# Performance work log

Measured on AMD Instinct MI355X. Metric: run time of the kernel, lower is better.

Reference implementation:

```python
import jax, jax.numpy as jnp
import numpy as np

N_HEAD = 16
N_KV_HEAD = 8
HEAD_DIM = 128
N_EMBED = 2048
EPS = 1.1920929e-07  # torch default eps for fp32 rms_norm


def _apply_rotary_emb(x, cos, sin):
    # x: (B, T, H, D); cos/sin: (1, T, 1, D//2)  (nanochat-style half rotation)
    d = x.shape[-1] // 2
    x1, x2 = x[..., :d], x[..., d:]
    y1 = x1 * cos + x2 * sin
    y2 = -x1 * sin + x2 * cos
    return jnp.concatenate([y1, y2], axis=-1).astype(x.dtype)


def _rms_norm(x):
    return x * jax.lax.rsqrt(jnp.mean(jnp.square(x), axis=-1, keepdims=True) + EPS)


def setup_inputs() -> dict:
    key = jax.random.key(0)
    ks = jax.random.split(key, 5)
    B, T = 2, 2048
    kv_dim = N_KV_HEAD * HEAD_DIM
    x = jax.random.normal(ks[0], (B, T, N_EMBED), dtype=jnp.float32)
    w_attn = jax.random.normal(ks[1], (N_EMBED + 2 * kv_dim, N_EMBED), dtype=jnp.float32) * 0.02
    w_proj = jax.random.normal(ks[2], (N_EMBED, N_EMBED), dtype=jnp.float32) * 0.02
    # realistic RoPE tables
    half = HEAD_DIM // 2
    inv_freq = 1.0 / (10000.0 ** (jnp.arange(half, dtype=jnp.float32) / half))
    freqs = jnp.arange(T, dtype=jnp.float32)[:, None] * inv_freq[None, :]  # (T, half)
    cos = jnp.cos(freqs)[None, :, None, :]
    sin = jnp.sin(freqs)[None, :, None, :]
    return {"x": x, "w_attn": w_attn, "w_proj": w_proj, "cos": cos, "sin": sin}


def reference(x, w_attn, w_proj, cos, sin):
    B, T, C = x.shape
    kv_dim = N_KV_HEAD * HEAD_DIM
    qkv = jnp.einsum('btc,oc->bto', x, w_attn)  # (B, T, C + 2*kv_dim)
    q = qkv[..., :C].reshape(B, T, N_HEAD, HEAD_DIM)
    k = qkv[..., C:C + kv_dim].reshape(B, T, N_KV_HEAD, HEAD_DIM)
    v = qkv[..., C + kv_dim:].reshape(B, T, N_KV_HEAD, HEAD_DIM)
    q = _rms_norm(_apply_rotary_emb(q, cos, sin))
    k = _rms_norm(_apply_rotary_emb(k, cos, sin))
    # GQA: repeat kv heads to match query heads
    rep = N_HEAD // N_KV_HEAD
    k = jnp.repeat(k, rep, axis=2)  # (B, T, n_head, D)
    v = jnp.repeat(v, rep, axis=2)
    scale = 1.0 / jnp.sqrt(jnp.float32(HEAD_DIM))
    scores = jnp.einsum('bqhd,bkhd->bhqk', q, k) * scale  # (B, H, T, T)
    causal = jnp.tril(jnp.ones((T, T), dtype=bool))
    scores = jnp.where(causal[None, None], scores, jnp.finfo(scores.dtype).min)
    attn = jax.nn.softmax(scores, axis=-1)
    y = jnp.einsum('bhqk,bkhd->bqhd', attn, v).reshape(B, T, C)
    return jnp.einsum('btc,oc->bto', y, w_proj)
```

## Files before the change

kernel.cpp:

```cpp
#include <hip/hip_runtime.h>

#define B_ 2
#define T_ 2048
#define NH 16
#define NKV 8
#define HD 128
#define C_ 2048
#define KVD (NKV*HD)
#define QKVD (C_ + 2*KVD)
#define NTOK (B_*T_)

typedef __bf16 bf16_t;
typedef __bf16 bf16x4_t __attribute__((ext_vector_type(4)));
typedef __bf16 bf16x8_t __attribute__((ext_vector_type(8)));
typedef float f32x4_t __attribute__((ext_vector_type(4)));
typedef float f32x16_t __attribute__((ext_vector_type(16)));

__device__ __forceinline__ f32x4_t mfma16(bf16x8_t a, bf16x8_t b, f32x4_t c) {
  return __builtin_amdgcn_mfma_f32_16x16x32_bf16(a, b, c, 0, 0, 0);
}
__device__ __forceinline__ f32x16_t mfma32(bf16x8_t a, bf16x8_t b, f32x16_t c) {
  return __builtin_amdgcn_mfma_f32_32x32x16_bf16(a, b, c, 0, 0, 0);
}
__device__ __forceinline__ f32x16_t zero16() {
  f32x16_t z;
  #pragma unroll
  for (int i = 0; i < 16; i++) z[i] = 0.f;
  return z;
}

#define GLDS16(gp, lp) __builtin_amdgcn_global_load_lds( \
    (const __attribute__((address_space(1))) void*)(gp), \
    (__attribute__((address_space(3))) void*)(lp), 16, 0, 0)

__global__ __launch_bounds__(256) void cvt3_kernel(const float* __restrict__ s0, bf16_t* __restrict__ d0,
                                                   const float* __restrict__ s1, bf16_t* __restrict__ d1,
                                                   const float* __restrict__ s2, bf16_t* __restrict__ d2) {
  int bid = blockIdx.x;
  const float* s; bf16_t* d; int off;
  if (bid < 8192)       { s = s0; d = d0; off = bid; }
  else if (bid < 16384) { s = s1; d = d1; off = bid - 8192; }
  else                  { s = s2; d = d2; off = bid - 16384; }
  int i = (off * 256 + threadIdx.x) * 4;
  const float4 v = *(const float4*)(s + i);
  bf16x4_t o;
  o[0] = (bf16_t)v.x; o[1] = (bf16_t)v.y; o[2] = (bf16_t)v.z; o[3] = (bf16_t)v.w;
  *(bf16x4_t*)(d + i) = o;
}

__global__ void gemm_nt(const bf16_t* __restrict__ A, const bf16_t* __restrict__ Bm,
                        float* __restrict__ Cf, bf16_t* __restrict__ Cb, int M, int N, int K) {
  __shared__ bf16_t As[128*32];
  __shared__ bf16_t Bs[128*32];
  int tid = threadIdx.x;
  int wave = tid >> 6, lane = tid & 63;
  int quad = lane >> 4, l16 = lane & 15;
  int wm = (wave >> 1) * 64, wn = (wave & 1) * 64;
  int bm = blockIdx.y * 128, bn = blockIdx.x * 128;
  int grow = wave * 32 + (lane >> 2);
  int gcol = (lane & 3) * 8;
  const bf16_t* pa = A + (size_t)(bm + grow) * K + gcol;
  const bf16_t* pb = Bm + (size_t)(bn + grow) * K + gcol;
  bf16_t* lA0 = &As[(wave * 32) * 32];
  bf16_t* lA1 = &As[(wave * 32 + 16) * 32];
  bf16_t* lB0 = &Bs[(wave * 32) * 32];
  bf16_t* lB1 = &Bs[(wave * 32 + 16) * 32];
  f32x4_t acc[4][4];
  #pragma unroll
  for (int i = 0; i < 4; i++)
    #pragma unroll
    for (int j = 0; j < 4; j++) acc[i][j] = (f32x4_t){0.f,0.f,0.f,0.f};
  for (int k0 = 0; k0 < K; k0 += 32) {
    __syncthreads();
    GLDS16(pa + k0, lA0);
    GLDS16(pa + (size_t)16 * K + k0, lA1);
    GLDS16(pb + k0, lB0);
    GLDS16(pb + (size_t)16 * K + k0, lB1);
    __syncthreads();
    bf16x8_t af[4], bfr[4];
    #pragma unroll
    for (int i = 0; i < 4; i++) {
      af[i]  = *(const bf16x8_t*)&As[(wm + i*16 + l16)*32 + quad*8];
      bfr[i] = *(const bf16x8_t*)&Bs[(wn + i*16 + l16)*32 + quad*8];
    }
    #pragma unroll
    for (int i = 0; i < 4; i++)
      #pragma unroll
      for (int j = 0; j < 4; j++)
        acc[i][j] = mfma16(af[i], bfr[j], acc[i][j]);
  }
  if (Cb) {
    #pragma unroll
    for (int i = 0; i < 4; i++)
      #pragma unroll
      for (int j = 0; j < 4; j++) {
        int row0 = bm + wm + i*16 + quad*4;
        int col  = bn + wn + j*16 + l16;
        #pragma unroll
        for (int r = 0; r < 4; r++)
          Cb[(size_t)(row0 + r) * N + col] = (bf16_t)acc[i][j][r];
      }
  } else {
    #pragma unroll
    for (int i = 0; i < 4; i++)
      #pragma unroll
      for (int j = 0; j < 4; j++) {
        int row0 = bm + wm + i*16 + quad*4;
        int col  = bn + wn + j*16 + l16;
        #pragma unroll
        for (int r = 0; r < 4; r++)
          Cf[(size_t)(row0 + r) * N + col] = acc[i][j][r];
      }
  }
}

__global__ __launch_bounds__(256) void rope_norm_kernel(const bf16_t* __restrict__ qkv,
    const float* __restrict__ cosb, const float* __restrict__ sinb,
    bf16_t* __restrict__ qb, bf16_t* __restrict__ kb) {
  int token = blockIdx.y;
  int slot = blockIdx.x * 4 + (threadIdx.x >> 6);
  int lane = threadIdx.x & 63;
  int b = token >> 11, s = token & 2047;
  const bf16_t* row = qkv + (size_t)token * QKVD;
  int base_in = (slot < 16) ? slot * HD : C_ + (slot - 16) * HD;
  float x1 = (float)row[base_in + lane];
  float x2 = (float)row[base_in + 64 + lane];
  float c = cosb[s*64 + lane], sn = sinb[s*64 + lane];
  float y1 = x1*c + x2*sn;
  float y2 = x2*c - x1*sn;
  float ss = y1*y1 + y2*y2;
  ss += __shfl_xor(ss, 1);  ss += __shfl_xor(ss, 2);  ss += __shfl_xor(ss, 4);
  ss += __shfl_xor(ss, 8);  ss += __shfl_xor(ss, 16); ss += __shfl_xor(ss, 32);
  float r = rsqrtf(ss * (1.0f/128.0f) + 1.1920929e-07f);
  bf16_t* dst;
  if (slot < 16) {
    r *= 0.08838834764831845f * 1.4426950408889634f;
    dst = qb + ((size_t)(b*NH + slot) * T_ + s) * HD;
  } else {
    dst = kb + ((size_t)(b*NKV + (slot-16)) * T_ + s) * HD;
  }
  dst[lane]      = (bf16_t)(y1 * r);
  dst[lane + 64] = (bf16_t)(y2 * r);
}

__global__ __launch_bounds__(256) void transpose_v(const bf16_t* __restrict__ qkv,
                                                   bf16_t* __restrict__ vt) {
  __shared__ bf16_t TT[64*136];
  int bk = blockIdx.y;
  int b = bk >> 3, kv = bk & 7;
  int s0 = blockIdx.x * 64;
  int tid = threadIdx.x;
  int row = tid >> 2, c0 = (tid & 3) * 32;
  const bf16_t* src = qkv + (size_t)(b*T_ + s0 + row) * QKVD + C_ + KVD + kv*HD + c0;
  #pragma unroll
  for (int s4 = 0; s4 < 4; s4++)
    *(bf16x8_t*)&TT[row*136 + c0 + s4*8] = *(const bf16x8_t*)(src + s4*8);
  __syncthreads();
  #pragma unroll
  for (int s2 = 0; s2 < 2; s2++) {
    int d = (tid >> 2) + s2*64;
    #pragma unroll
    for (int s = 0; s < 2; s++) {
      int g = (tid & 3) * 8 + s*32;
      bf16x8_t pk;
      #pragma unroll
      for (int e = 0; e < 8; e++) pk[e] = TT[(g + e)*136 + d];
      *(bf16x8_t*)(vt + ((size_t)bk * HD + d) * T_ + s0 + g) = pk;
    }
  }
}

__global__ __launch_bounds__(256, 2) void attn_kernel(const bf16_t* __restrict__ qb,
    const bf16_t* __restrict__ kb, const bf16_t* __restrict__ vt, bf16_t* __restrict__ yb) {
  __shared__ bf16_t Ks[64*136];
  __shared__ bf16_t Vs[128*72];
  __shared__ bf16_t Ps[4][32*72];
  int L = blockIdx.x;
  int s = (L >> 8) & 1;
  int bh = (L >> 3) & 31;
  int qt = s ? (15 - 2*(L & 7)) : (2*(L & 7));
  int b = bh >> 4, h = bh & 15, kvh = h >> 1;
  int tid = threadIdx.x, wave = tid >> 6, lane = tid & 63;
  int l32 = lane & 31, half = lane >> 5;
  const bf16_t* Qp = qb + (size_t)bh * T_ * HD;
  const bf16_t* Kp = kb + (size_t)(b*NKV + kvh) * T_ * HD;
  const bf16_t* Vt = vt + (size_t)(b*NKV + kvh) * HD * T_;

  int qrow = qt*128 + wave*32 + l32;
  bf16x8_t qf[8];
  #pragma unroll
  for (int kc = 0; kc < 8; kc++)
    qf[kc] = *(const bf16x8_t*)(Qp + (size_t)qrow * HD + kc*16 + half*8);

  float mrow = -1e30f, lrow = 0.f;
  f32x16_t o[4];
  #pragma unroll
  for (int mb = 0; mb < 4; mb++) o[mb] = zero16();

  int krow = tid >> 2, kcb = (tid & 3) * 32;
  int vd = tid >> 1,  vcb = (tid & 1) * 32;

  int nkt = 2*qt + 2;
  for (int kt = 0; kt < nkt; kt++) {
    int k0 = kt * 64;
    __syncthreads();
    {
      const bf16_t* src = Kp + (size_t)(k0 + krow) * HD + kcb;
      #pragma unroll
      for (int ss2 = 0; ss2 < 4; ss2++)
        *(bf16x8_t*)&Ks[krow*136 + kcb + ss2*8] = *(const bf16x8_t*)(src + ss2*8);
    }
    {
      const bf16_t* src = Vt + (size_t)vd * T_ + k0 + vcb;
      #pragma unroll
      for (int ss2 = 0; ss2 < 4; ss2++)
        *(bf16x8_t*)&Vs[vd*72 + vcb + ss2*8] = *(const bf16x8_t*)(src + ss2*8);
    }
    __syncthreads();

    f32x16_t sacc[2];
    sacc[0] = zero16(); sacc[1] = zero16();
    #pragma unroll
    for (int kc = 0; kc < 8; kc++) {
      #pragma unroll
      for (int mb = 0; mb < 2; mb++) {
        bf16x8_t kf = *(const bf16x8_t*)&Ks[(mb*32 + l32)*136 + kc*16 + half*8];
        sacc[mb] = mfma32(kf, qf[kc], sacc[mb]);
      }
    }
    if (k0 + 63 > qt*128 + wave*32) {
      #pragma unroll
      for (int mb = 0; mb < 2; mb++)
        #pragma unroll
        for (int r = 0; r < 16; r++) {
          int key = k0 + mb*32 + (r&3) + 8*(r>>2) + 4*half;
          if (key > qrow) sacc[mb][r] = -1e30f;
        }
    }
    float mx = -1e30f;
    #pragma unroll
    for (int mb = 0; mb < 2; mb++)
      #pragma unroll
      for (int r = 0; r < 16; r++) mx = fmaxf(mx, sacc[mb][r]);
    mx = fmaxf(mx, __shfl_xor(mx, 32));
    float mnew = fmaxf(mrow, mx);
    float alpha = exp2f(mrow - mnew);
    mrow = mnew;
    float rs = 0.f;
    #pragma unroll
    for (int mb = 0; mb < 2; mb++)
      #pragma unroll
      for (int r = 0; r < 16; r++) {
        float p = exp2f(sacc[mb][r] - mnew);
        sacc[mb][r] = p;
        rs += p;
      }
    rs += __shfl_xor(rs, 32);
    lrow = lrow * alpha + rs;
    #pragma unroll
    for (int mb = 0; mb < 4; mb++) o[mb] = o[mb] * alpha;
    #pragma unroll
    for (int mb = 0; mb < 2; mb++)
      #pragma unroll
      for (int rr = 0; rr < 4; rr++) {
        bf16x4_t pk;
        pk[0] = (bf16_t)sacc[mb][rr*4+0]; pk[1] = (bf16_t)sacc[mb][rr*4+1];
        pk[2] = (bf16_t)sacc[mb][rr*4+2]; pk[3] = (bf16_t)sacc[mb][rr*4+3];
        *(bf16x4_t*)&Ps[wave][l32*72 + mb*32 + rr*8 + half*4] = pk;
      }
    bf16x8_t pf[4];
    #pragma unroll
    for (int kc = 0; kc < 4; kc++)
      pf[kc] = *(const bf16x8_t*)&Ps[wave][l32*72 + kc*16 + half*8];
    #pragma unroll
    for (int mb = 0; mb < 4; mb++)
      #pragma unroll
      for (int kc = 0; kc < 4; kc++) {
        bf16x8_t vf = *(const bf16x8_t*)&Vs[(mb*32 + l32)*72 + kc*16 + half*8];
        o[mb] = mfma32(vf, pf[kc], o[mb]);
      }
  }
  __syncthreads();
  bf16_t* OL = (wave < 2) ? &Ks[wave * 4352] : &Vs[(wave - 2) * 4352];
  float invl = 1.0f / lrow;
  #pragma unroll
  for (int mb = 0; mb < 4; mb++)
    #pragma unroll
    for (int rr = 0; rr < 4; rr++) {
      bf16x4_t pk;
      pk[0] = (bf16_t)(o[mb][rr*4+0] * invl); pk[1] = (bf16_t)(o[mb][rr*4+1] * invl);
      pk[2] = (bf16_t)(o[mb][rr*4+2] * invl); pk[3] = (bf16_t)(o[mb][rr*4+3] * invl);
      *(bf16x4_t*)&OL[l32*136 + mb*32 + rr*8 + half*4] = pk;
    }
  int row = l32, seg = half;
  int tok = qt*128 + wave*32 + row;
  bf16_t* dst = yb + ((size_t)(b*T_ + tok) * NH + h) * HD + seg*64;
  #pragma unroll
  for (int j = 0; j < 8; j++)
    *(bf16x8_t*)(dst + j*8) = *(const bf16x8_t*)&OL[row*136 + seg*64 + j*8];
}

extern "C" void kernel_launch(void* const* d_in, const int* in_sizes, int n_in,
                              void* d_out, int out_size, void* d_ws, size_t ws_size,
                              hipStream_t stream) {
  const float* x      = (const float*)d_in[0];
  const float* w_attn = (const float*)d_in[1];
  const float* w_proj = (const float*)d_in[2];
  const float* cosb   = (const float*)d_in[3];
  const float* sinb   = (const float*)d_in[4];
  float* out = (float*)d_out;

  bf16_t* xb   = (bf16_t*)d_ws;
  bf16_t* wab  = xb + 8388608;
  bf16_t* wpb  = wab + 8388608;
  bf16_t* qkvb = wpb + 4194304;
  bf16_t* qb   = qkvb + 16777216;
  bf16_t* kb   = qb + 8388608;
  bf16_t* vt   = kb + 4194304;
  bf16_t* yb   = vt + 4194304;

  cvt3_kernel<<<20480, 256, 0, stream>>>(x, xb, w_attn, wab, w_proj, wpb);

  gemm_nt<<<dim3(32, 32), 256, 0, stream>>>(xb, wab, nullptr, qkvb, NTOK, QKVD, C_);

  rope_norm_kernel<<<dim3(6, 4096), 256, 0, stream>>>(qkvb, cosb, sinb, qb, kb);
  transpose_v<<<dim3(32, 16), 256, 0, stream>>>(qkvb, vt);

  attn_kernel<<<512, 256, 0, stream>>>(qb, kb, vt, yb);

  gemm_nt<<<dim3(16, 32), 256, 0, stream>>>(yb, wpb, out, nullptr, NTOK, C_, C_);
}
```

Before: 353.9 us.

## Double-buffer K/V tiles, pair causal q-tiles per block, shuffle P in registers

Each attention block now handles two query tiles (j and 15-j) in sequence so causal work is balanced per block. K/V tiles are double-buffered in shared memory, with the next tile prefetched into registers while the current one is computed. The P matrix is rearranged into MFMA operand layout with cross-half lane shuffles instead of a round trip through shared memory. The risks are higher register pressure from the prefetch registers and half as many blocks in the grid, unless the launch size was changed as well.

Measured after the change: 453.6 us. 28.2% more time.

```diff
diff --git a/kernel.cpp b/kernel.cpp
--- a/kernel.cpp
+++ b/kernel.cpp
@@ -11,10 +11,12 @@
 #define NTOK (B_*T_)
 
 typedef __bf16 bf16_t;
+typedef __bf16 bf16x2_t __attribute__((ext_vector_type(2)));
 typedef __bf16 bf16x4_t __attribute__((ext_vector_type(4)));
 typedef __bf16 bf16x8_t __attribute__((ext_vector_type(8)));
 typedef float f32x4_t __attribute__((ext_vector_type(4)));
 typedef float f32x16_t __attribute__((ext_vector_type(16)));
+typedef int i32x4_t __attribute__((ext_vector_type(4)));
 
 __device__ __forceinline__ f32x4_t mfma16(bf16x8_t a, bf16x8_t b, f32x4_t c) {
   return __builtin_amdgcn_mfma_f32_16x16x32_bf16(a, b, c, 0, 0, 0);
@@ -27,6 +29,10 @@
   #pragma unroll
   for (int i = 0; i < 16; i++) z[i] = 0.f;
   return z;
+}
+__device__ __forceinline__ int pk2(float a, float b) {
+  bf16x2_t t; t[0] = (bf16_t)a; t[1] = (bf16_t)b;
+  return __builtin_bit_cast(int, t);
 }
 
 #define GLDS16(gp, lp) __builtin_amdgcn_global_load_lds( \
@@ -172,13 +178,11 @@
 
 __global__ __launch_bounds__(256, 2) void attn_kernel(const bf16_t* __restrict__ qb,
     const bf16_t* __restrict__ kb, const bf16_t* __restrict__ vt, bf16_t* __restrict__ yb) {
-  __shared__ bf16_t Ks[64*136];
-  __shared__ bf16_t Vs[128*72];
-  __shared__ bf16_t Ps[4][32*72];
+  __shared__ bf16_t Ksb[2][64*136];
+  __shared__ bf16_t Vsb[2][128*72];
   int L = blockIdx.x;
-  int s = (L >> 8) & 1;
-  int bh = (L >> 3) & 31;
-  int qt = s ? (15 - 2*(L & 7)) : (2*(L & 7));
+  int bh = L & 31;
+  int j = (L >> 5) & 15;
   int b = bh >> 4, h = bh & 15, kvh = h >> 1;
   int tid = threadIdx.x, wave = tid >> 6, lane = tid & 63;
   int l32 = lane & 31, half = lane >> 5;
@@ -186,118 +190,137 @@
   const bf16_t* Kp = kb + (size_t)(b*NKV + kvh) * T_ * HD;
   const bf16_t* Vt = vt + (size_t)(b*NKV + kvh) * HD * T_;
 
-  int qrow = qt*128 + wave*32 + l32;
-  bf16x8_t qf[8];
-  #pragma unroll
-  for (int kc = 0; kc < 8; kc++)
-    qf[kc] = *(const bf16x8_t*)(Qp + (size_t)qrow * HD + kc*16 + half*8);
-
-  float mrow = -1e30f, lrow = 0.f;
-  f32x16_t o[4];
-  #pragma unroll
-  for (int mb = 0; mb < 4; mb++) o[mb] = zero16();
-
   int krow = tid >> 2, kcb = (tid & 3) * 32;
   int vd = tid >> 1,  vcb = (tid & 1) * 32;
 
-  int nkt = 2*qt + 2;
-  for (int kt = 0; kt < nkt; kt++) {
-    int k0 = kt * 64;
-    __syncthreads();
+  #pragma unroll
+  for (int ph = 0; ph < 2; ph++) {
+    int qt = ph ? (15 - j) : j;
+    int qrow = qt*128 + wave*32 + l32;
+    bf16x8_t qf[8];
+    #pragma unroll
+    for (int kc = 0; kc < 8; kc++)
+      qf[kc] = *(const bf16x8_t*)(Qp + (size_t)qrow * HD + kc*16 + half*8);
+
+    float mrow = -1e30f, lrow = 0.f;
+    f32x16_t o[4];
+    #pragma unroll
+    for (int mb = 0; mb < 4; mb++) o[mb] = zero16();
+
+    int nkt = 2*qt + 2;
+    bf16x8_t kreg[4], vreg[4];
     {
-      const bf16_t* src = Kp + (size_t)(k0 + krow) * HD + kcb;
-      #pragma unroll
-      for (int ss2 = 0; ss2 < 4; ss2++)
-        *(bf16x8_t*)&Ks[krow*136 + kcb + ss2*8] = *(const bf16x8_t*)(src + ss2*8);
-    }
-    {
-      const bf16_t* src = Vt + (size_t)vd * T_ + k0 + vcb;
-      #pragma unroll
-      for (int ss2 = 0; ss2 < 4; ss2++)
-        *(bf16x8_t*)&Vs[vd*72 + vcb + ss2*8] = *(const bf16x8_t*)(src + ss2*8);
+      const bf16_t* srck = Kp + (size_t)krow * HD + kcb;
+      const bf16_t* srcv = Vt + (size_t)vd * T_ + vcb;
+      #pragma unroll
+      for (int s2 = 0; s2 < 4; s2++) { kreg[s2] = *(const bf16x8_t*)(srck + s2*8);
+                                       vreg[s2] = *(const bf16x8_t*)(srcv + s2*8); }
     }
     __syncthreads();
-
-    f32x16_t sacc[2];
-    sacc[0] = zero16(); sacc[1] = zero16();
-    #pragma unroll
-    for (int kc = 0; kc < 8; kc++) {
-      #pragma unroll
-      for (int mb = 0; mb < 2; mb++) {
-        bf16x8_t kf = *(const bf16x8_t*)&Ks[(mb*32 + l32)*136 + kc*16 + half*8];
-        sacc[mb] = mfma32(kf, qf[kc], sacc[mb]);
+    #pragma unroll
+    for (int s2 = 0; s2 < 4; s2++) { *(bf16x8_t*)&Ksb[0][krow*136 + kcb + s2*8] = kreg[s2];
+                                     *(bf16x8_t*)&Vsb[0][vd*72   + vcb + s2*8] = vreg[s2]; }
+
+    for (int kt = 0; kt < nkt; kt++) {
+      __syncthreads();
+      int cur = kt & 1;
+      if (kt + 1 < nkt) {
+        int k1 = (kt + 1) * 64;
+        const bf16_t* srck = Kp + (size_t)(k1 + krow) * HD + kcb;
+        const bf16_t* srcv = Vt + (size_t)vd * T_ + k1 + vcb;
+        #pragma unroll
+        for (int s2 = 0; s2 < 4; s2++) { kreg[s2] = *(const bf16x8_t*)(srck + s2*8);
+                                         vreg[s2] = *(const bf16x8_t*)(srcv + s2*8); }
+      }
+      int k0 = kt * 64;
+      f32x16_t sacc[2];
+      sacc[0] = zero16(); sacc[1] = zero16();
+      #pragma unroll
+      for (int kc = 0; kc < 8; kc++)
+        #pragma unroll
+        for (int mb = 0; mb < 2; mb++) {
+          bf16x8_t kf = *(const bf16x8_t*)&Ksb[cur][(mb*32 + l32)*136 + kc*16 + half*8];
+          sacc[mb] = mfma32(kf, qf[kc], sacc[mb]);
+        }
+      if (k0 + 63 > qt*128 + wave*32) {
+        #pragma unroll
+        for (int mb = 0; mb < 2; mb++)
+          #pragma unroll
+          for (int r = 0; r < 16; r++) {
+            int key = k0 + mb*32 + (r&3) + 8*(r>>2) + 4*half;
+            if (key > qrow) sacc[mb][r] = -1e30f;
+          }
+      }
+      float mx = -1e30f;
+      #pragma unroll
+      for (int mb = 0; mb < 2; mb++)
+        #pragma unroll
+        for (int r = 0; r < 16; r++) mx = fmaxf(mx, sacc[mb][r]);
+      mx = fmaxf(mx, __shfl_xor(mx, 32));
+      float mnew = fmaxf(mrow, mx);
+      float alpha = exp2f(mrow - mnew);
+      mrow = mnew;
+      float rs = 0.f;
+      #pragma unroll
+      for (int mb = 0; mb < 2; mb++)
+        #pragma unroll
+        for (int r = 0; r < 16; r++) {
+          float p = exp2f(sacc[mb][r] - mnew);
+          sacc[mb][r] = p;
+          rs += p;
+        }
+      rs += __shfl_xor(rs, 32);
+      lrow = lrow * alpha + rs;
+      #pragma unroll
+      for (int mb = 0; mb < 4; mb++) o[mb] = o[mb] * alpha;
+      int Lpk[2][4], Rpk[2][4];
+      #pragma unroll
+      for (int mb = 0; mb < 2; mb++)
+        #pragma unroll
+        for (int d = 0; d < 4; d++) {
+          int base = 2*d + ((d >= 2) ? 4 : 0);
+          Lpk[mb][d] = pk2(sacc[mb][base + 4*half],     sacc[mb][base + 1 + 4*half]);
+          int spk    = pk2(sacc[mb][base + 4*(1-half)], sacc[mb][base + 1 + 4*(1-half)]);
+          Rpk[mb][d] = __shfl_xor(spk, 32);
+        }
+      #pragma unroll
+      for (int kc = 0; kc < 4; kc++) {
+        int mb = kc >> 1, q2 = (kc & 1) * 2;
+        int x0 = Lpk[mb][q2], x1 = Lpk[mb][q2+1], y0 = Rpk[mb][q2], y1 = Rpk[mb][q2+1];
+        i32x4_t wv;
+        wv[0] = half ? y0 : x0; wv[1] = half ? y1 : x1;
+        wv[2] = half ? x0 : y0; wv[3] = half ? x1 : y1;
+        bf16x8_t pf = __builtin_bit_cast(bf16x8_t, wv);
+        #pragma unroll
+        for (int mbd = 0; mbd < 4; mbd++) {
+          bf16x8_t vf = *(const bf16x8_t*)&Vsb[cur][(mbd*32 + l32)*72 + kc*16 + half*8];
+          o[mbd] = mfma32(vf, pf, o[mbd]);
+        }
+      }
+      if (kt + 1 < nkt) {
+        #pragma unroll
+        for (int s2 = 0; s2 < 4; s2++) { *(bf16x8_t*)&Ksb[1-cur][krow*136 + kcb + s2*8] = kreg[s2];
+                                         *(bf16x8_t*)&Vsb[1-cur][vd*72   + vcb + s2*8] = vreg[s2]; }
       }
     }
-    if (k0 + 63 > qt*128 + wave*32) {
-      #pragma unroll
-      for (int mb = 0; mb < 2; mb++)
-        #pragma unroll
-        for (int r = 0; r < 16; r++) {
-          int key = k0 + mb*32 + (r&3) + 8*(r>>2) + 4*half;
-          if (key > qrow) sacc[mb][r] = -1e30f;
-        }
-    }
-    float mx = -1e30f;
-    #pragma unroll
-    for (int mb = 0; mb < 2; mb++)
-      #pragma unroll
-      for (int r = 0; r < 16; r++) mx = fmaxf(mx, sacc[mb][r]);
-    mx = fmaxf(mx, __shfl_xor(mx, 32));
-    float mnew = fmaxf(mrow, mx);
-    float alpha = exp2f(mrow - mnew);
-    mrow = mnew;
-    float rs = 0.f;
-    #pragma unroll
-    for (int mb = 0; mb < 2; mb++)
-      #pragma unroll
-      for (int r = 0; r < 16; r++) {
-        float p = exp2f(sacc[mb][r] - mnew);
-        sacc[mb][r] = p;
-        rs += p;
-      }
-    rs += __shfl_xor(rs, 32);
-    lrow = lrow * alpha + rs;
-    #pragma unroll
-    for (int mb = 0; mb < 4; mb++) o[mb] = o[mb] * alpha;
-    #pragma unroll
-    for (int mb = 0; mb < 2; mb++)
+    __syncthreads();
+    bf16_t* OL = (wave < 2) ? &Ksb[0][wave * 4352] : &Ksb[1][(wave - 2) * 4352];
+    float invl = 1.0f / lrow;
+    #pragma unroll
+    for (int mb = 0; mb < 4; mb++)
       #pragma unroll
       for (int rr = 0; rr < 4; rr++) {
         bf16x4_t pk;
-        pk[0] = (bf16_t)sacc[mb][rr*4+0]; pk[1] = (bf16_t)sacc[mb][rr*4+1];
-        pk[2] = (bf16_t)sacc[mb][rr*4+2]; pk[3] = (bf16_t)sacc[mb][rr*4+3];
-        *(bf16x4_t*)&Ps[wave][l32*72 + mb*32 + rr*8 + half*4] = pk;
-      }
-    bf16x8_t pf[4];
-    #pragma unroll
-    for (int kc = 0; kc < 4; kc++)
-      pf[kc] = *(const bf16x8_t*)&Ps[wave][l32*72 + kc*16 + half*8];
-    #pragma unroll
-    for (int mb = 0; mb < 4; mb++)
-      #pragma unroll
-      for (int kc = 0; kc < 4; kc++) {
-        bf16x8_t vf = *(const bf16x8_t*)&Vs[(mb*32 + l32)*72 + kc*16 + half*8];
-        o[mb] = mfma32(vf, pf[kc], o[mb]);
-      }
-  }
-  __syncthreads();
-  bf16_t* OL = (wave < 2) ? &Ks[wave * 4352] : &Vs[(wave - 2) * 4352];
-  float invl = 1.0f / lrow;
-  #pragma unroll
-  for (int mb = 0; mb < 4; mb++)
-    #pragma unroll
-    for (int rr = 0; rr < 4; rr++) {
-      bf16x4_t pk;
-      pk[0] = (bf16_t)(o[mb][rr*4+0] * invl); pk[1] = (bf16_t)(o[mb][rr*4+1] * invl);
-      pk[2] = (bf16_t)(o[mb][rr*4+2] * invl); pk[3] = (bf16_t)(o[mb][rr*4+3] * invl);
-      *(bf16x4_t*)&OL[l32*136 + mb*32 + rr*8 + half*4] = pk;
-    }
-  int row = l32, seg = half;
-  int tok = qt*128 + wave*32 + row;
-  bf16_t* dst = yb + ((size_t)(b*T_ + tok) * NH + h) * HD + seg*64;
-  #pragma unroll
-  for (int j = 0; j < 8; j++)
-    *(bf16x8_t*)(dst + j*8) = *(const bf16x8_t*)&OL[row*136 + seg*64 + j*8];
+        pk[0] = (bf16_t)(o[mb][rr*4+0] * invl); pk[1] = (bf16_t)(o[mb][rr*4+1] * invl);
+        pk[2] = (bf16_t)(o[mb][rr*4+2] * invl); pk[3] = (bf16_t)(o[mb][rr*4+3] * invl);
+        *(bf16x4_t*)&OL[l32*136 + mb*32 + rr*8 + half*4] = pk;
+      }
+    int tok = qt*128 + wave*32 + l32;
+    bf16_t* dst = yb + ((size_t)(b*T_ + tok) * NH + h) * HD + half*64;
+    #pragma unroll
+    for (int jj = 0; jj < 8; jj++)
+      *(bf16x8_t*)(dst + jj*8) = *(const bf16x8_t*)&OL[l32*136 + half*64 + jj*8];
+  }
 }
 
 extern "C" void kernel_launch(void* const* d_in, const int* in_sizes, int n_in,
```
